# Kernel tuning notes

Hardware: AMD Instinct MI355X
Metric: run time of the kernel (lower is better)

The kernel has to match this reference:

```python
import jax, jax.numpy as jnp
import numpy as np

NH, NOPE, ROPE, VD, KVL = 16, 128, 64, 128, 512
QHD = NOPE + ROPE  # 192
EPS = 1e-6
THETA = 10000.0


def rmsnorm(x, w):
    v = jnp.mean(x.astype(jnp.float32) ** 2, axis=-1, keepdims=True)
    return w * (x * jax.lax.rsqrt(v + EPS)).astype(x.dtype)


def _interleave_perm(x):
    # x.view(..., d//2, 2).transpose(-1, -2).reshape(..., d): [x0,x2,...,x1,x3,...]
    return jnp.concatenate([x[..., 0::2], x[..., 1::2]], axis=-1)


def _rotate_half(x):
    d = x.shape[-1] // 2
    return jnp.concatenate([-x[..., d:], x[..., :d]], axis=-1)


def _rope(x, cos, sin):
    x = _interleave_perm(x)
    return x * cos + _rotate_half(x) * sin


def reference(hidden_states, position_ids, q_a_w, q_a_ln, q_b_w, kv_a_w, kv_a_ln, kv_b_w, o_w):
    B, S, _ = hidden_states.shape
    h = hidden_states

    # low-rank Q: q_b(rmsnorm(q_a(h)))
    q = rmsnorm(h @ q_a_w.T, q_a_ln) @ q_b_w.T          # [B,S,NH*192]
    q = q.reshape(B, S, NH, QHD).transpose(0, 2, 1, 3)   # [B,NH,S,192]
    q_nope, q_pe = q[..., :NOPE], q[..., NOPE:]

    # compressed KV + shared rope key
    ckv = h @ kv_a_w.T                                    # [B,S,KVL+ROPE]
    compressed, k_pe = ckv[..., :KVL], ckv[..., KVL:]
    k_pe = k_pe.reshape(B, S, 1, ROPE).transpose(0, 2, 1, 3)  # [B,1,S,ROPE]

    kv = rmsnorm(compressed, kv_a_ln) @ kv_b_w.T          # [B,S,NH*(NOPE+VD)]
    kv = kv.reshape(B, S, NH, NOPE + VD).transpose(0, 2, 1, 3)
    k_nope, v = kv[..., :NOPE], kv[..., NOPE:]            # [B,NH,S,*]

    # rotary cache
    inv_freq = 1.0 / (THETA ** (jnp.arange(0, ROPE, 2, dtype=jnp.float32) / ROPE))
    t = jnp.arange(S, dtype=jnp.float32)
    freqs = jnp.outer(t, inv_freq)
    emb = jnp.concatenate([freqs, freqs], axis=-1)        # [S,ROPE]
    cos = jnp.cos(emb)[position_ids][:, None]             # [B,1,S,ROPE]
    sin = jnp.sin(emb)[position_ids][:, None]

    q_pe = _rope(q_pe, cos, sin)
    k_pe = _rope(k_pe, cos, sin)

    query = jnp.concatenate([q_nope, q_pe], axis=-1)                       # [B,NH,S,192]
    key = jnp.concatenate([k_nope, jnp.broadcast_to(k_pe, (B, NH, S, ROPE))], axis=-1)

    scale = QHD ** -0.5
    scores = jnp.einsum('bhqd,bhkd->bhqk', query, key) * scale
    causal = jnp.tril(jnp.ones((S, S), dtype=bool))
    scores = jnp.where(causal, scores, jnp.finfo(scores.dtype).min)
    attn = jax.nn.softmax(scores.astype(jnp.float32), axis=-1).astype(query.dtype)

    out = jnp.einsum('bhqk,bhkd->bhqd', attn, v)          # [B,NH,S,VD]
    out = out.transpose(0, 2, 1, 3).reshape(B, S, NH * VD)
    return out @ o_w.T


def setup_inputs():
    key = jax.random.key(0)
    ks = jax.random.split(key, 7)
    B, S, HID, QL = 2, 1024, 2048, 1536
    w = lambda i, shape: jax.random.normal(ks[i], shape, jnp.float32) / np.sqrt(shape[-1])
    return {
        'hidden_states': jax.random.normal(ks[0], (B, S, HID), jnp.float32),
        'position_ids': jnp.tile(jnp.arange(S, dtype=jnp.int32)[None, :], (B, 1)),
        'q_a_w': w(1, (QL, HID)),
        'q_a_ln': jnp.ones((QL,), jnp.float32),
        'q_b_w': w(2, (NH * QHD, QL)),
        'kv_a_w': w(3, (KVL + ROPE, HID)),
        'kv_a_ln': jnp.ones((KVL,), jnp.float32),
        'kv_b_w': w(4, (NH * (NOPE + VD), KVL)),
        'o_w': w(5, (HID, NH * VD)),
    }
```

## Files before the change

kernel.cpp:

```cpp
#include <hip/hip_runtime.h>
#include <stdint.h>
#include <math.h>

typedef unsigned short u16;
typedef __attribute__((ext_vector_type(8))) short short8;
typedef __attribute__((ext_vector_type(4))) short short4v;
typedef __attribute__((ext_vector_type(4))) float f32x4;

#define DEVFN static __device__ __forceinline__

DEVFN float bf2f(short b) {
  union { unsigned int i; float f; } u;
  u.i = ((unsigned int)(unsigned short)b) << 16;
  return u.f;
}
DEVFN short f2bf(float f) {
  union { float f; unsigned int i; } u; u.f = f;
  unsigned int r = u.i + 0x7fffu + ((u.i >> 16) & 1u);
  return (short)(r >> 16);
}

DEVFN f32x4 mfma32(short8 a, short8 b, f32x4 c) {
  return __builtin_amdgcn_mfma_f32_16x16x32_bf16(a, b, c, 0, 0, 0);
}
DEVFN f32x4 mfma16(short4v a, short4v b, f32x4 c) {
#if defined(__HIP_DEVICE_COMPILE__)
  return __builtin_amdgcn_mfma_f32_16x16x16bf16_1k(a, b, c, 0, 0, 0);
#else
  (void)a; (void)b; return c;
#endif
}

typedef const __attribute__((address_space(1))) unsigned int* gp_t;
typedef __attribute__((address_space(3))) unsigned int* lp_t;
typedef const __attribute__((address_space(3))) u16* lds_cp;
DEVFN void async_copy16(u16* lds, const u16* g) {
  __builtin_amdgcn_global_load_lds((gp_t)(const void*)g, (lp_t)(void*)lds, 16, 0, 0);
}
DEVFN short4v tr_read16(const u16* p) {
  short4v r;
  asm volatile("ds_read_b64_tr_b16 %0, %1" : "=v"(r) : "v"((lds_cp)(const void*)p));
  return r;
}
DEVFN void raw_barrier() {
  asm volatile("" ::: "memory");
  __builtin_amdgcn_s_barrier();
  asm volatile("" ::: "memory");
}

__global__ void cast_kernel(const float* __restrict__ in, u16* __restrict__ out, int n4) {
  int i = blockIdx.x * blockDim.x + threadIdx.x;
  if (i < n4) {
    f32x4 v = ((const f32x4*)in)[i];
    short4v o;
    o[0] = f2bf(v[0]); o[1] = f2bf(v[1]); o[2] = f2bf(v[2]); o[3] = f2bf(v[3]);
    ((short4v*)out)[i] = o;
  }
}

__global__ void cast5_kernel(const float* __restrict__ s0, const float* __restrict__ s1,
                             const float* __restrict__ s2, const float* __restrict__ s3,
                             const float* __restrict__ s4,
                             u16* __restrict__ d0, u16* __restrict__ d1,
                             u16* __restrict__ d2, u16* __restrict__ d3,
                             u16* __restrict__ d4) {
  int i = blockIdx.x * blockDim.x + threadIdx.x;
  const float* s; u16* d; int off;
  if (i < 1048576)      { s = s0; d = d0; off = 0; }
  else if (i < 1835008) { s = s1; d = d1; off = 1048576; }
  else if (i < 2129920) { s = s2; d = d2; off = 1835008; }
  else if (i < 3309568) { s = s3; d = d3; off = 2129920; }
  else                  { s = s4; d = d4; off = 3309568; }
  int j = i - off;
  f32x4 v = ((const f32x4*)s)[j];
  short4v o;
  o[0] = f2bf(v[0]); o[1] = f2bf(v[1]); o[2] = f2bf(v[2]); o[3] = f2bf(v[3]);
  ((short4v*)d)[j] = o;
}

__global__ void rmsnorm_kernel(const u16* __restrict__ in, int istride,
                               u16* __restrict__ out, int ostride,
                               const float* __restrict__ w, int len) {
  const int row = blockIdx.x, t = threadIdx.x;
  short8 v = *(const short8*)(in + (size_t)row * istride + t * 8);
  float f[8]; float ss = 0.f;
#pragma unroll
  for (int j = 0; j < 8; ++j) { f[j] = bf2f(v[j]); ss += f[j] * f[j]; }
#pragma unroll
  for (int off = 1; off < 64; off <<= 1) ss += __shfl_xor(ss, off);
  __shared__ float red[8];
  int nw = (int)blockDim.x >> 6;
  if ((t & 63) == 0) red[t >> 6] = ss;
  __syncthreads();
  ss = 0.f;
  for (int i = 0; i < nw; ++i) ss += red[i];
  float r = rsqrtf(ss / (float)len + 1e-6f);
  const float* wp = w + t * 8;
  short8 ov;
#pragma unroll
  for (int j = 0; j < 8; ++j) ov[j] = f2bf(f[j] * r * wp[j]);
  *(short8*)(out + (size_t)row * ostride + t * 8) = ov;
}

__global__ void rope_kernel(const u16* __restrict__ q, const u16* __restrict__ ckv,
                            int cstride,
                            const int* __restrict__ pos_ids,
                            u16* __restrict__ qpe, u16* __restrict__ kpe) {
  const int row = blockIdx.x;
  const int t = threadIdx.x;
  const float pos = (float)pos_ids[row];
  const float L2TH = 13.287712379549449f;
  if (t < 32) {
    int i = t;
    float inv = exp2f(-L2TH * (float)i / 32.0f);
    float sv, cv; sincosf(pos * inv, &sv, &cv);
    float x0 = bf2f(ckv[(size_t)row * cstride + 512 + 2 * i]);
    float x1 = bf2f(ckv[(size_t)row * cstride + 512 + 2 * i + 1]);
    kpe[(size_t)row * 64 + i]      = (u16)f2bf(x0 * cv - x1 * sv);
    kpe[(size_t)row * 64 + 32 + i] = (u16)f2bf(x1 * cv + x0 * sv);
  }
#pragma unroll
  for (int j = 0; j < 8; ++j) {
    int idx = t + 64 * j;
    int hh = idx >> 5, i = idx & 31;
    float inv = exp2f(-L2TH * (float)i / 32.0f);
    float sv, cv; sincosf(pos * inv, &sv, &cv);
    const u16* base = q + (size_t)row * 3072 + hh * 192 + 128;
    float x0 = bf2f(base[2 * i]), x1 = bf2f(base[2 * i + 1]);
    u16* ob = qpe + ((size_t)row * 16 + hh) * 64;
    ob[i]      = (u16)f2bf(x0 * cv - x1 * sv);
    ob[32 + i] = (u16)f2bf(x1 * cv + x0 * sv);
  }
}

template <int BM, int BN, bool OUT_F32, int TAG>
__global__ __launch_bounds__(256) void gemm_bt(const u16* __restrict__ A,
                                               const u16* __restrict__ B,
                                               void* __restrict__ C,
                                               int M, int N, int K, int ldc) {
  constexpr int ACH = BM / 32;
  constexpr int BCH = BN / 32;
  constexpr int MI  = BM / 32;
  constexpr int NI  = BN / 32;
  constexpr int LOADS = ACH + BCH;
  __shared__ u16 As[2][BM * 64];
  __shared__ u16 Bs[2][BN * 64];
  const int tid = threadIdx.x;
  const int w = tid >> 6, l = tid & 63;
  const int lq = l & 15, lg = l >> 4;
  const int wm = (w >> 1) * (BM / 2);
  const int wn = (w & 1) * (BN / 2);

  const int f = blockIdx.x + gridDim.x * blockIdx.y;
  const int nwg = gridDim.x * gridDim.y;
  const int swz = (f & 7) * (nwg >> 3) + (f >> 3);
  const int bx = swz % gridDim.x, by = swz / gridDim.x;
  const int m0 = by * BM, n0 = bx * BN;

  const u16* srcA[ACH]; int dstA[ACH];
#pragma unroll
  for (int i = 0; i < ACH; ++i) {
    int c = i * 256 + tid;
    int row = c >> 3, pc = c & 7;
    int lc = pc ^ (row & 7);
    srcA[i] = A + (size_t)(m0 + row) * K + lc * 8;
    dstA[i] = c * 8;
  }
  const u16* srcB[BCH]; int dstB[BCH];
#pragma unroll
  for (int i = 0; i < BCH; ++i) {
    int c = i * 256 + tid;
    int row = c >> 3, pc = c & 7;
    int lc = pc ^ (row & 7);
    srcB[i] = B + (size_t)(n0 + row) * K + lc * 8;
    dstB[i] = c * 8;
  }

  auto stage = [&](int buf) {
#pragma unroll
    for (int i = 0; i < ACH; ++i) {
      async_copy16(&As[buf][dstA[i]], srcA[i]);
      srcA[i] += 64;
    }
#pragma unroll
    for (int i = 0; i < BCH; ++i) {
      async_copy16(&Bs[buf][dstB[i]], srcB[i]);
      srcB[i] += 64;
    }
  };

  f32x4 acc[MI][NI];
#pragma unroll
  for (int i = 0; i < MI; ++i)
#pragma unroll
    for (int j = 0; j < NI; ++j) acc[i][j] = (f32x4){0.f, 0.f, 0.f, 0.f};

  const int nt = K >> 6;
  stage(0);
  if (nt > 1) stage(1);

  for (int t = 0; t < nt; ++t) {
    if (t + 1 < nt) {
      if constexpr (LOADS == 4)      asm volatile("s_waitcnt vmcnt(4)" ::: "memory");
      else if constexpr (LOADS == 6) asm volatile("s_waitcnt vmcnt(6)" ::: "memory");
      else if constexpr (LOADS == 7) asm volatile("s_waitcnt vmcnt(7)" ::: "memory");
      else                           asm volatile("s_waitcnt vmcnt(8)" ::: "memory");
    } else {
      asm volatile("s_waitcnt vmcnt(0)" ::: "memory");
    }
    raw_barrier();

    const int buf = t & 1;
#pragma unroll
    for (int ks = 0; ks < 2; ++ks) {
      short8 af[MI], bfr[NI];
#pragma unroll
      for (int mi = 0; mi < MI; ++mi) {
        int row = wm + mi * 16 + lq;
        int ch = ((ks << 2) | lg) ^ (row & 7);
        af[mi] = *(const short8*)&As[buf][row * 64 + ch * 8];
      }
#pragma unroll
      for (int ni = 0; ni < NI; ++ni) {
        int row = wn + ni * 16 + lq;
        int ch = ((ks << 2) | lg) ^ (row & 7);
        bfr[ni] = *(const short8*)&Bs[buf][row * 64 + ch * 8];
      }
#pragma unroll
      for (int mi = 0; mi < MI; ++mi)
#pragma unroll
        for (int ni = 0; ni < NI; ++ni)
          acc[mi][ni] = mfma32(af[mi], bfr[ni], acc[mi][ni]);
    }

    raw_barrier();
    if (t + 2 < nt) stage(buf);
  }

#pragma unroll
  for (int mi = 0; mi < MI; ++mi) {
#pragma unroll
    for (int ni = 0; ni < NI; ++ni) {
      int col = n0 + wn + ni * 16 + lq;
#pragma unroll
      for (int r = 0; r < 4; ++r) {
        int rowm = m0 + wm + mi * 16 + lg * 4 + r;
        if constexpr (OUT_F32)
          ((float*)C)[(size_t)rowm * ldc + col] = acc[mi][ni][r];
        else
          ((u16*)C)[(size_t)rowm * ldc + col] = (u16)f2bf(acc[mi][ni][r]);
      }
    }
  }
}

__global__ __launch_bounds__(512, 4) void attn_kernel(const u16* __restrict__ q,
                                                      const u16* __restrict__ qpe,
                                                      const u16* __restrict__ kv,
                                                      const u16* __restrict__ kpe,
                                                      u16* __restrict__ o) {
  __shared__ u16 Ks[2][2][32 * 192];
  __shared__ u16 Vs[2][2][32 * 128];
  const int S = 1024;
  const int tid = threadIdx.x;
  const int w = tid >> 6, l = tid & 63;
  const int team = w >> 2, wt = w & 3;
  const int lq = l & 15, lg = l >> 4;
  const int h = blockIdx.y, b = blockIdx.z;
  const int chunk = b ? (15 - (int)blockIdx.x) : (int)blockIdx.x;
  const int q0 = chunk * 64 + wt * 16;
  const int nkt = chunk + 1;
  const size_t qrow = (size_t)b * S + q0 + lq;

  short8 qf[6];
#pragma unroll
  for (int c = 0; c < 4; ++c)
    qf[c] = *(const short8*)(q + qrow * 3072 + h * 192 + c * 32 + lg * 8);
#pragma unroll
  for (int c = 0; c < 2; ++c)
    qf[4 + c] = *(const short8*)(qpe + (qrow * 16 + h) * 64 + c * 32 + lg * 8);

  const size_t gb = (size_t)b * S + 32 * team;
  const u16* srcK[3]; int strK[3];
#pragma unroll
  for (int j = 0; j < 3; ++j) {
    int n = wt * 192 + j * 64 + l;
    int row = (n * 2731) >> 16;
    int pc = n - row * 24;
    int lc = (pc & ~7) | ((pc & 7) ^ (row & 7));
    if (lc < 16) { srcK[j] = kv + (gb + row) * 4096 + h * 256 + lc * 8; strK[j] = 64 * 4096; }
    else         { srcK[j] = kpe + (gb + row) * 64 + (lc - 16) * 8;     strK[j] = 64 * 64; }
  }
  const u16* srcV[2];
#pragma unroll
  for (int j = 0; j < 2; ++j) {
    int n = wt * 128 + j * 64 + l;
    int dsub = n >> 6, m = n & 63;
    int ksub = m >> 3, r = (m >> 1) & 3, half = m & 1;
    srcV[j] = kv + (gb + ksub * 4 + r) * 4096 + h * 256 + 128 + dsub * 16 + half * 8;
  }

  auto stage = [&](int buf) {
#pragma unroll
    for (int j = 0; j < 3; ++j) {
      async_copy16(&Ks[buf][team][(wt * 192 + j * 64) * 8], srcK[j]);
      srcK[j] += strK[j];
    }
#pragma unroll
    for (int j = 0; j < 2; ++j) {
      async_copy16(&Vs[buf][team][(wt * 128 + j * 64) * 8], srcV[j]);
      srcV[j] += 64 * 4096;
    }
  };

  const float scl = 0.07216878364870323f * 1.4426950408889634f;
  float m2 = -INFINITY, lsum = 0.f;
  f32x4 oac[8];
#pragma unroll
  for (int dt = 0; dt < 8; ++dt) oac[dt] = (f32x4){0.f, 0.f, 0.f, 0.f};

  const int e0 = (lg ^ (lq & 7)) << 4;
  const int vbase = lg * 64 + lq * 4;

  stage(0);
  asm volatile("s_waitcnt vmcnt(0)" ::: "memory");
  __syncthreads();

  int buf = 0;
  for (int i = 0; i < nkt; ++i) {
    if (i + 1 < nkt) stage(buf ^ 1);
    const int kbase = (2 * i + team) * 32;

    if (kbase <= q0 + 15) {
      const char* kb = (const char*)&Ks[buf][team][0];
      f32x4 sac0, sac1;
#pragma unroll
      for (int kt2 = 0; kt2 < 2; ++kt2) {
        int a0 = (kt2 * 16 + lq) * 384 + e0;
        int a1 = a0 ^ 64;
        f32x4 s = (f32x4){0.f, 0.f, 0.f, 0.f};
        s = mfma32(*(const short8*)(kb + a0),       qf[0], s);
        s = mfma32(*(const short8*)(kb + a1),       qf[1], s);
        s = mfma32(*(const short8*)(kb + a0 + 128), qf[2], s);
        s = mfma32(*(const short8*)(kb + a1 + 128), qf[3], s);
        s = mfma32(*(const short8*)(kb + a0 + 256), qf[4], s);
        s = mfma32(*(const short8*)(kb + a1 + 256), qf[5], s);
        if (kt2 == 0) sac0 = s; else sac1 = s;
      }

      const int qi = q0 + lq;
      const int kb0 = kbase + lg * 4;
      float s2[8];
#pragma unroll
      for (int r = 0; r < 4; ++r) {
        s2[r]     = (kb0 + r      <= qi) ? sac0[r] * scl : -INFINITY;
        s2[4 + r] = (kb0 + 16 + r <= qi) ? sac1[r] * scl : -INFINITY;
      }
      float mt = fmaxf(fmaxf(fmaxf(s2[0], s2[1]), fmaxf(s2[2], s2[3])),
                       fmaxf(fmaxf(s2[4], s2[5]), fmaxf(s2[6], s2[7])));
      mt = fmaxf(mt, __shfl_xor(mt, 16));
      mt = fmaxf(mt, __shfl_xor(mt, 32));
      float mnew = fmaxf(m2, mt);
      float resc = exp2f(m2 - mnew);
      float psum = 0.f;
#pragma unroll
      for (int r = 0; r < 8; ++r) { s2[r] = exp2f(s2[r] - mnew); psum += s2[r]; }
      psum += __shfl_xor(psum, 16);
      psum += __shfl_xor(psum, 32);
      lsum = lsum * resc + psum;
      m2 = mnew;
      short4v pf0, pf1;
#pragma unroll
      for (int r = 0; r < 4; ++r) { pf0[r] = f2bf(s2[r]); pf1[r] = f2bf(s2[4 + r]); }

#pragma unroll
      for (int hf = 0; hf < 2; ++hf) {
        short4v vf[4][2];
#pragma unroll
        for (int dd = 0; dd < 4; ++dd)
#pragma unroll
          for (int kt2 = 0; kt2 < 2; ++kt2)
            vf[dd][kt2] = tr_read16(&Vs[buf][team][vbase + (hf * 4 + dd) * 512 + kt2 * 256]);
        asm volatile("s_waitcnt lgkmcnt(0)" ::: "memory");
        __builtin_amdgcn_sched_barrier(0);
#pragma unroll
        for (int dd = 0; dd < 4; ++dd) {
          const int dt = hf * 4 + dd;
          f32x4 t = oac[dt];
          t[0] *= resc; t[1] *= resc; t[2] *= resc; t[3] *= resc;
          t = mfma16(vf[dd][0], pf0, t);
          t = mfma16(vf[dd][1], pf1, t);
          oac[dt] = t;
        }
      }
    }

    asm volatile("s_waitcnt vmcnt(0)" ::: "memory");
    __syncthreads();
    buf ^= 1;
  }

  float* MO = (float*)&Ks[0][0][0];
  float* MS = (float*)&Vs[0][0][0];
  const int qr = wt * 16 + lq;
  if (team == 1) {
#pragma unroll
    for (int dt = 0; dt < 8; ++dt)
#pragma unroll
      for (int r = 0; r < 4; ++r)
        MO[qr * 129 + dt * 16 + lg * 4 + r] = oac[dt][r];
    if (lg == 0) { MS[qr * 2] = m2; MS[qr * 2 + 1] = lsum; }
  }
  __syncthreads();
  if (team == 0) {
    float m1 = MS[qr * 2], l1 = MS[qr * 2 + 1];
    float mn = fmaxf(m2, m1);
    float a0 = exp2f(m2 - mn), a1 = exp2f(m1 - mn);
    float inv = 1.f / (lsum * a0 + l1 * a1);
#pragma unroll
    for (int dt = 0; dt < 8; ++dt)
#pragma unroll
      for (int r = 0; r < 4; ++r) {
        float val = (oac[dt][r] * a0 + MO[qr * 129 + dt * 16 + lg * 4 + r] * a1) * inv;
        o[((size_t)b * S + q0 + lq) * 2048 + h * 128 + dt * 16 + lg * 4 + r] = (u16)f2bf(val);
      }
  }
}

extern "C" void kernel_launch(void* const* d_in, const int* in_sizes, int n_in,
                              void* d_out, int out_size, void* d_ws, size_t ws_size,
                              hipStream_t stream) {
  const float* h_in  = (const float*)d_in[0];
  const int*   pos   = (const int*)d_in[1];
  const float* qaw   = (const float*)d_in[2];
  const float* qaln  = (const float*)d_in[3];
  const float* qbw   = (const float*)d_in[4];
  const float* kvaw  = (const float*)d_in[5];
  const float* kvaln = (const float*)d_in[6];
  const float* kvbw  = (const float*)d_in[7];
  const float* ow    = (const float*)d_in[8];
  float* out = (float*)d_out;

  const int M = 2048;
  char* p = (char*)d_ws;
  auto alloc = [&](size_t bytes) {
    char* r = p;
    p += (bytes + 255) & ~(size_t)255;
    return (u16*)r;
  };
  u16* h_bf   = alloc((size_t)M * 2048 * 2);
  u16* Wfused = alloc((size_t)2112 * 2048 * 2);
  u16* Wqb    = alloc((size_t)3072 * 1536 * 2);
  u16* Wkvb   = alloc((size_t)4096 * 512 * 2);
  u16* F      = alloc((size_t)M * 2112 * 2);
  u16* qbuf   = alloc((size_t)M * 3072 * 2);
  u16* kvb    = alloc((size_t)M * 4096 * 2);
  u16* qpe    = alloc((size_t)M * 16 * 64 * 2);
  u16* kpe    = alloc((size_t)M * 64 * 2);
  u16* qa    = Wfused;
  u16* ckvn  = Wfused + (size_t)1536 * 2048;
  u16* attno = h_bf;
  u16* OW    = qbuf;

  dim3 blk(256);

  cast5_kernel<<<14976, blk, 0, stream>>>(h_in, qaw, kvaw, qbw, kvbw,
                                          h_bf, Wfused, Wfused + (size_t)1536 * 2048,
                                          Wqb, Wkvb);

  gemm_bt<128, 64, false, 1><<<dim3(33, 16), blk, 0, stream>>>(h_bf, Wfused, F, M, 2112, 2048, 2112);
  rmsnorm_kernel<<<2048, 192, 0, stream>>>(F, 2112, qa, 1536, qaln, 1536);
  rmsnorm_kernel<<<2048, 64, 0, stream>>>(F + 1536, 2112, ckvn, 512, kvaln, 512);

  gemm_bt<128, 96, false, 2><<<dim3(32, 16), blk, 0, stream>>>(qa, Wqb, qbuf, M, 3072, 1536, 3072);

  gemm_bt<128, 128, false, 4><<<dim3(32, 16), blk, 0, stream>>>(ckvn, Wkvb, kvb, M, 4096, 512, 4096);

  rope_kernel<<<2048, 64, 0, stream>>>(qbuf, F + 1536, 2112, pos, qpe, kpe);

  attn_kernel<<<dim3(16, 16, 2), 512, 0, stream>>>(qbuf, qpe, kvb, kpe, attno);

  cast_kernel<<<4096, blk, 0, stream>>>(ow, OW, 1048576);
  gemm_bt<128, 64, true, 5><<<dim3(32, 16), blk, 0, stream>>>(attno, OW, out, M, 2048, 2048, 2048);
}
```

Baseline: 171.1 us.

## Fuse casts and rmsnorm launches, add triple-buffered output projection GEMM

Folds the o_w weight cast into the combined cast kernel, using a dedicated buffer instead of reusing qbuf, so one launch disappears. Merges the two rmsnorm launches into a single kernel with 4096 blocks of 192 threads, where idle threads skip work for the KV rows. Replaces the final output GEMM with a new triple-buffered variant that issues the next tile's async loads before waiting. These target launch overhead and memory latency, at the cost of more workspace and extra shared memory for the third buffer.

```diff
diff --git a/kernel.cpp b/kernel.cpp
--- a/kernel.cpp
+++ b/kernel.cpp
@@ -48,29 +48,20 @@
   asm volatile("" ::: "memory");
 }
 
-__global__ void cast_kernel(const float* __restrict__ in, u16* __restrict__ out, int n4) {
-  int i = blockIdx.x * blockDim.x + threadIdx.x;
-  if (i < n4) {
-    f32x4 v = ((const f32x4*)in)[i];
-    short4v o;
-    o[0] = f2bf(v[0]); o[1] = f2bf(v[1]); o[2] = f2bf(v[2]); o[3] = f2bf(v[3]);
-    ((short4v*)out)[i] = o;
-  }
-}
-
-__global__ void cast5_kernel(const float* __restrict__ s0, const float* __restrict__ s1,
+__global__ void cast6_kernel(const float* __restrict__ s0, const float* __restrict__ s1,
                              const float* __restrict__ s2, const float* __restrict__ s3,
-                             const float* __restrict__ s4,
+                             const float* __restrict__ s4, const float* __restrict__ s5,
                              u16* __restrict__ d0, u16* __restrict__ d1,
                              u16* __restrict__ d2, u16* __restrict__ d3,
-                             u16* __restrict__ d4) {
+                             u16* __restrict__ d4, u16* __restrict__ d5) {
   int i = blockIdx.x * blockDim.x + threadIdx.x;
   const float* s; u16* d; int off;
   if (i < 1048576)      { s = s0; d = d0; off = 0; }
   else if (i < 1835008) { s = s1; d = d1; off = 1048576; }
   else if (i < 2129920) { s = s2; d = d2; off = 1835008; }
   else if (i < 3309568) { s = s3; d = d3; off = 2129920; }
-  else                  { s = s4; d = d4; off = 3309568; }
+  else if (i < 3833856) { s = s4; d = d4; off = 3309568; }
+  else                  { s = s5; d = d5; off = 3833856; }
   int j = i - off;
   f32x4 v = ((const f32x4*)s)[j];
   short4v o;
@@ -78,28 +69,39 @@
   ((short4v*)d)[j] = o;
 }
 
-__global__ void rmsnorm_kernel(const u16* __restrict__ in, int istride,
-                               u16* __restrict__ out, int ostride,
-                               const float* __restrict__ w, int len) {
-  const int row = blockIdx.x, t = threadIdx.x;
-  short8 v = *(const short8*)(in + (size_t)row * istride + t * 8);
+__global__ void rmsnorm2_kernel(const u16* __restrict__ F,
+                                const float* __restrict__ qln,
+                                const float* __restrict__ kvln,
+                                u16* __restrict__ qa, u16* __restrict__ ckvn) {
+  const int bid = blockIdx.x, t = threadIdx.x;
+  const bool isQ = bid < 2048;
+  const int row = isQ ? bid : bid - 2048;
+  const u16* in = (isQ ? F : F + 1536) + (size_t)row * 2112;
+  u16* out = isQ ? (qa + (size_t)row * 1536) : (ckvn + (size_t)row * 512);
+  const float* w = isQ ? qln : kvln;
+  const int len = isQ ? 1536 : 512;
+  const int nact = len >> 3;
   float f[8]; float ss = 0.f;
-#pragma unroll
-  for (int j = 0; j < 8; ++j) { f[j] = bf2f(v[j]); ss += f[j] * f[j]; }
+  short8 v = {};
+  if (t < nact) {
+    v = *(const short8*)(in + t * 8);
+#pragma unroll
+    for (int j = 0; j < 8; ++j) { f[j] = bf2f(v[j]); ss += f[j] * f[j]; }
+  }
 #pragma unroll
   for (int off = 1; off < 64; off <<= 1) ss += __shfl_xor(ss, off);
-  __shared__ float red[8];
-  int nw = (int)blockDim.x >> 6;
+  __shared__ float red[3];
   if ((t & 63) == 0) red[t >> 6] = ss;
   __syncthreads();
-  ss = 0.f;
-  for (int i = 0; i < nw; ++i) ss += red[i];
+  ss = red[0] + red[1] + red[2];
   float r = rsqrtf(ss / (float)len + 1e-6f);
-  const float* wp = w + t * 8;
-  short8 ov;
-#pragma unroll
-  for (int j = 0; j < 8; ++j) ov[j] = f2bf(f[j] * r * wp[j]);
-  *(short8*)(out + (size_t)row * ostride + t * 8) = ov;
+  if (t < nact) {
+    const float* wp = w + t * 8;
+    short8 ov;
+#pragma unroll
+    for (int j = 0; j < 8; ++j) ov[j] = f2bf(bf2f(v[j]) * r * wp[j]);
+    *(short8*)(out + t * 8) = ov;
+  }
 }
 
 __global__ void rope_kernel(const u16* __restrict__ q, const u16* __restrict__ ckv,
@@ -254,6 +256,122 @@
   }
 }
 
+template <int BM, int BN, bool OUT_F32, int TAG>
+__global__ __launch_bounds__(256) void gemm_bt3(const u16* __restrict__ A,
+                                                const u16* __restrict__ B,
+                                                void* __restrict__ C,
+                                                int M, int N, int K, int ldc) {
+  constexpr int ACH = BM / 32;
+  constexpr int BCH = BN / 32;
+  constexpr int MI  = BM / 32;
+  constexpr int NI  = BN / 32;
+  constexpr int LOADS = ACH + BCH;
+  static_assert(LOADS == 6, "pilot sized for BM128/BN64");
+  __shared__ u16 As[3][BM * 64];
+  __shared__ u16 Bs[3][BN * 64];
+  const int tid = threadIdx.x;
+  const int w = tid >> 6, l = tid & 63;
+  const int lq = l & 15, lg = l >> 4;
+  const int wm = (w >> 1) * (BM / 2);
+  const int wn = (w & 1) * (BN / 2);
+
+  const int f = blockIdx.x + gridDim.x * blockIdx.y;
+  const int nwg = gridDim.x * gridDim.y;
+  const int swz = (f & 7) * (nwg >> 3) + (f >> 3);
+  const int bx = swz % gridDim.x, by = swz / gridDim.x;
+  const int m0 = by * BM, n0 = bx * BN;
+
+  const u16* srcA[ACH]; int dstA[ACH];
+#pragma unroll
+  for (int i = 0; i < ACH; ++i) {
+    int c = i * 256 + tid;
+    int row = c >> 3, pc = c & 7;
+    int lc = pc ^ (row & 7);
+    srcA[i] = A + (size_t)(m0 + row) * K + lc * 8;
+    dstA[i] = c * 8;
+  }
+  const u16* srcB[BCH]; int dstB[BCH];
+#pragma unroll
+  for (int i = 0; i < BCH; ++i) {
+    int c = i * 256 + tid;
+    int row = c >> 3, pc = c & 7;
+    int lc = pc ^ (row & 7);
+    srcB[i] = B + (size_t)(n0 + row) * K + lc * 8;
+    dstB[i] = c * 8;
+  }
+
+  auto stage = [&](int buf) {
+#pragma unroll
+    for (int i = 0; i < ACH; ++i) {
+      async_copy16(&As[buf][dstA[i]], srcA[i]);
+      srcA[i] += 64;
+    }
+#pragma unroll
+    for (int i = 0; i < BCH; ++i) {
+      async_copy16(&Bs[buf][dstB[i]], srcB[i]);
+      srcB[i] += 64;
+    }
+  };
+
+  f32x4 acc[MI][NI];
+#pragma unroll
+  for (int i = 0; i < MI; ++i)
+#pragma unroll
+    for (int j = 0; j < NI; ++j) acc[i][j] = (f32x4){0.f, 0.f, 0.f, 0.f};
+
+  const int nt = K >> 6;
+  stage(0);
+
+  for (int t = 0; t < nt; ++t) {
+    if (t + 1 < nt) {
+      stage((t + 1) % 3);
+      asm volatile("s_waitcnt vmcnt(6)" ::: "memory");
+    } else {
+      asm volatile("s_waitcnt vmcnt(0)" ::: "memory");
+    }
+    raw_barrier();
+
+    const int buf = t % 3;
+#pragma unroll
+    for (int ks = 0; ks < 2; ++ks) {
+      short8 af[MI], bfr[NI];
+#pragma unroll
+      for (int mi = 0; mi < MI; ++mi) {
+        int row = wm + mi * 16 + lq;
+        int ch = ((ks << 2) | lg) ^ (row & 7);
+        af[mi] = *(const short8*)&As[buf][row * 64 + ch * 8];
+      }
+#pragma unroll
+      for (int ni = 0; ni < NI; ++ni) {
+        int row = wn + ni * 16 + lq;
+        int ch = ((ks << 2) | lg) ^ (row & 7);
+        bfr[ni] = *(const short8*)&Bs[buf][row * 64 + ch * 8];
+      }
+#pragma unroll
+      for (int mi = 0; mi < MI; ++mi)
+#pragma unroll
+        for (int ni = 0; ni < NI; ++ni)
+          acc[mi][ni] = mfma32(af[mi], bfr[ni], acc[mi][ni]);
+    }
+  }
+
+#pragma unroll
+  for (int mi = 0; mi < MI; ++mi) {
+#pragma unroll
+    for (int ni = 0; ni < NI; ++ni) {
+      int col = n0 + wn + ni * 16 + lq;
+#pragma unroll
+      for (int r = 0; r < 4; ++r) {
+        int rowm = m0 + wm + mi * 16 + lg * 4 + r;
+        if constexpr (OUT_F32)
+          ((float*)C)[(size_t)rowm * ldc + col] = acc[mi][ni][r];
+        else
+          ((u16*)C)[(size_t)rowm * ldc + col] = (u16)f2bf(acc[mi][ni][r]);
+      }
+    }
+  }
+}
+
 __global__ __launch_bounds__(512, 4) void attn_kernel(const u16* __restrict__ q,
                                                       const u16* __restrict__ qpe,
                                                       const u16* __restrict__ kv,
@@ -452,6 +570,7 @@
   u16* Wfused = alloc((size_t)2112 * 2048 * 2);
   u16* Wqb    = alloc((size_t)3072 * 1536 * 2);
   u16* Wkvb   = alloc((size_t)4096 * 512 * 2);
+  u16* OW     = alloc((size_t)2048 * 2048 * 2);
   u16* F      = alloc((size_t)M * 2112 * 2);
   u16* qbuf   = alloc((size_t)M * 3072 * 2);
   u16* kvb    = alloc((size_t)M * 4096 * 2);
@@ -460,17 +579,16 @@
   u16* qa    = Wfused;
   u16* ckvn  = Wfused + (size_t)1536 * 2048;
   u16* attno = h_bf;
-  u16* OW    = qbuf;
 
   dim3 blk(256);
 
-  cast5_kernel<<<14976, blk, 0, stream>>>(h_in, qaw, kvaw, qbw, kvbw,
+  cast6_kernel<<<19072, blk, 0, stream>>>(h_in, qaw, kvaw, qbw, kvbw, ow,
                                           h_bf, Wfused, Wfused + (size_t)1536 * 2048,
-                                          Wqb, Wkvb);
+                                          Wqb, Wkvb, OW);
 
   gemm_bt<128, 64, false, 1><<<dim3(33, 16), blk, 0, stream>>>(h_bf, Wfused, F, M, 2112, 2048, 2112);
-  rmsnorm_kernel<<<2048, 192, 0, stream>>>(F, 2112, qa, 1536, qaln, 1536);
-  rmsnorm_kernel<<<2048, 64, 0, stream>>>(F + 1536, 2112, ckvn, 512, kvaln, 512);
+
+  rmsnorm2_kernel<<<4096, 192, 0, stream>>>(F, qaln, kvaln, qa, ckvn);
 
   gemm_bt<128, 96, false, 2><<<dim3(32, 16), blk, 0, stream>>>(qa, Wqb, qbuf, M, 3072, 1536, 3072);
 
@@ -480,6 +598,5 @@
 
   attn_kernel<<<dim3(16, 16, 2), 512, 0, stream>>>(qbuf, qpe, kvb, kpe, attno);
 
-  cast_kernel<<<4096, blk, 0, stream>>>(ow, OW, 1048576);
-  gemm_bt<128, 64, true, 5><<<dim3(32, 16), blk, 0, stream>>>(attno, OW, out, M, 2048, 2048, 2048);
-}
+  gemm_bt3<128, 64, true, 5><<<dim3(32, 16), blk, 0, stream>>>(attno, OW, out, M, 2048, 2048, 2048);
+}
```

Result: faster. 167.2 us (-2.3%).
